# Performance work log

Hardware: AMD Instinct MI355X
Metric: run time of the kernel (lower is better)

## Reference

```python
import jax, jax.numpy as jnp
import numpy as np

_ALPHA_EPS = 1e-6


def _ema_weight_matrices(raw_alpha, T, dtype):
    """Return (K, T, T) row-normalized causal EMA weight matrices.

    W[k, t, s] = alpha_k^(t-s) / Z_t for s <= t, else 0, with Z_t the row sum.
    Computed in log space exactly like the torch reference.
    """
    alpha = jax.nn.sigmoid(raw_alpha).astype(dtype)
    alpha_safe = jnp.clip(alpha, _ALPHA_EPS, 1.0 - _ALPHA_EPS)  # (K,)
    idx = jnp.arange(T, dtype=dtype)
    diffs = idx[:, None] - idx[None, :]          # (T, T), t - s
    causal = diffs >= 0
    log_alpha = jnp.log(alpha_safe)              # (K,)
    log_W = log_alpha[:, None, None] * jnp.maximum(diffs, 0.0)  # (K, T, T)
    neg_inf = jnp.array(-jnp.inf, dtype=dtype)
    log_W = jnp.where(causal[None, :, :], log_W, neg_inf)
    log_Z = jax.nn.logsumexp(log_W, axis=2, keepdims=True)      # (K, T, 1)
    return jnp.exp(log_W - log_Z)                # (K, T, T)


def setup_inputs() -> dict:
    key = jax.random.key(0)
    k1, k2 = jax.random.split(key)
    B, T, d, K = 4, 4096, 512, 4
    h = jax.random.normal(k1, (B, T, d), dtype=jnp.float32)
    raw_alpha = jax.random.normal(k2, (K,), dtype=jnp.float32)
    return {"h": h, "raw_alpha": raw_alpha}


def reference(h, raw_alpha):
    """h: (B, T, d), raw_alpha: (K,) -> xis: (B, T, K, d)."""
    T = h.shape[1]
    W = _ema_weight_matrices(raw_alpha, T, h.dtype)   # (K, T, T)
    # per-channel causal weighted EMA: xi[b,t,k,:] = sum_s W[k,t,s] * h[b,s,:]
    return jnp.einsum('kts,bsd->btkd', W, h)
```

## Files before the change

### kernel.cpp

```cpp
#include <hip/hip_runtime.h>
#include <math.h>


namespace {

constexpr int T_LEN  = 4096;
constexpr int D_DIM  = 512;
constexpr int D4     = D_DIM / 4;
constexpr int K_CH   = 4;
constexpr int CHUNK  = 16;
constexpr int NCHUNK = T_LEN / CHUNK;
constexpr int GRP    = 16;
constexpr int NGRP   = NCHUNK / GRP;

typedef float floatx4 __attribute__((ext_vector_type(4)));

__device__ __forceinline__ float sigmoid_clip(float x) {
    float a = 1.0f / (1.0f + expf(-x));
    return fminf(fmaxf(a, 1e-6f), 1.0f - 1e-6f);
}

__device__ __forceinline__ void fma4(float4& d, float a, const float4& x) {
    d.x = fmaf(a, d.x, x.x);
    d.y = fmaf(a, d.y, x.y);
    d.z = fmaf(a, d.z, x.z);
    d.w = fmaf(a, d.w, x.w);
}

__device__ __forceinline__ void nt_store4(float4* p, const float4& v) {
    floatx4 nv;
    nv.x = v.x; nv.y = v.y; nv.z = v.z; nv.w = v.w;
    __builtin_nontemporal_store(nv, reinterpret_cast<floatx4*>(p));
}

__global__ void __launch_bounds__(128)
ema_chunk_sums(const float4* __restrict__ h4,
               const float*  __restrict__ raw_alpha,
               float4* __restrict__ lbuf) {
    const int c  = blockIdx.x % NCHUNK;
    const int b  = blockIdx.x / NCHUNK;
    const int d4 = threadIdx.x;

    float al[K_CH];
#pragma unroll
    for (int k = 0; k < K_CH; ++k) al[k] = sigmoid_clip(raw_alpha[k]);

    float4 acc[K_CH];
#pragma unroll
    for (int k = 0; k < K_CH; ++k) acc[k] = make_float4(0.f, 0.f, 0.f, 0.f);

    const float4* hp = h4 + ((size_t)b * T_LEN + (size_t)c * CHUNK) * D4 + d4;
#pragma unroll 4
    for (int j = 0; j < CHUNK; ++j) {
        const float4 hv = hp[(size_t)j * D4];
#pragma unroll
        for (int k = 0; k < K_CH; ++k) fma4(acc[k], al[k], hv);
    }
#pragma unroll
    for (int k = 0; k < K_CH; ++k)
        lbuf[(((size_t)b * NCHUNK + c) * K_CH + k) * D4 + d4] = acc[k];
}

__global__ void __launch_bounds__(128)
ema_group_sums(const float*  __restrict__ raw_alpha,
               const float4* __restrict__ lbuf,
               float4* __restrict__ gbuf) {
    const int g  = blockIdx.x % NGRP;
    const int b  = blockIdx.x / NGRP;
    const int d4 = threadIdx.x;

    float aC[K_CH];
#pragma unroll
    for (int k = 0; k < K_CH; ++k) {
        const float a = sigmoid_clip(raw_alpha[k]);
        aC[k] = exp2f((float)CHUNK * log2f(a));
    }

    float4 G[K_CH];
#pragma unroll
    for (int k = 0; k < K_CH; ++k) G[k] = make_float4(0.f, 0.f, 0.f, 0.f);

    const float4* lp = lbuf + (((size_t)b * NCHUNK + (size_t)g * GRP) * K_CH) * D4 + d4;
#pragma unroll 4
    for (int i = 0; i < GRP; ++i) {
#pragma unroll
        for (int k = 0; k < K_CH; ++k) {
            const float4 Lv = lp[((size_t)i * K_CH + k) * D4];
            fma4(G[k], aC[k], Lv);
        }
    }
#pragma unroll
    for (int k = 0; k < K_CH; ++k)
        gbuf[(((size_t)b * NGRP + g) * K_CH + k) * D4 + d4] = G[k];
}

__global__ void __launch_bounds__(128)
ema_apply(const float4* __restrict__ h4,
          const float*  __restrict__ raw_alpha,
          const float4* __restrict__ lbuf,
          const float4* __restrict__ gbuf,
          float4* __restrict__ out4) {
    const int c  = (NCHUNK - 1) - (blockIdx.x % NCHUNK);
    const int b  = blockIdx.x / NCHUNK;
    const int d4 = threadIdx.x;
    const int t0 = c * CHUNK;

    float al[K_CH], aC[K_CH], aG[K_CH];
#pragma unroll
    for (int k = 0; k < K_CH; ++k) {
        al[k] = sigmoid_clip(raw_alpha[k]);
        const float l2a = log2f(al[k]);
        aC[k] = exp2f((float)CHUNK * l2a);
        aG[k] = exp2f((float)(CHUNK * GRP) * l2a);
    }

    float4 S[K_CH];
#pragma unroll
    for (int k = 0; k < K_CH; ++k) S[k] = make_float4(0.f, 0.f, 0.f, 0.f);
    {
        const int g = c / GRP;
        const float4* gp = gbuf + ((size_t)b * NGRP * K_CH) * D4 + d4;
#pragma unroll 4
        for (int gq = 0; gq < g; ++gq) {
#pragma unroll
            for (int k = 0; k < K_CH; ++k) {
                const float4 Gv = gp[((size_t)gq * K_CH + k) * D4];
                fma4(S[k], aG[k], Gv);
            }
        }
        const float4* lp = lbuf + ((size_t)b * NCHUNK * K_CH) * D4 + d4;
#pragma unroll 4
        for (int cp = g * GRP; cp < c; ++cp) {
#pragma unroll
            for (int k = 0; k < K_CH; ++k) {
                const float4 Lv = lp[((size_t)cp * K_CH + k) * D4];
                fma4(S[k], aC[k], Lv);
            }
        }
    }

    float om[K_CH], pw[K_CH];
#pragma unroll
    for (int k = 0; k < K_CH; ++k) {
        om[k] = 1.0f - al[k];
        pw[k] = exp2f((float)(t0 + 1) * log2f(al[k]));
    }

    const float4* hp = h4 + ((size_t)b * T_LEN + t0) * D4 + d4;
    float4* op = out4 + (((size_t)b * T_LEN + t0) * (size_t)K_CH) * D4 + d4;

#pragma unroll 2
    for (int j = 0; j < CHUNK; ++j) {
        const float4 hv = hp[(size_t)j * D4];
#pragma unroll
        for (int k = 0; k < K_CH; ++k) {
            fma4(S[k], al[k], hv);
            const float invZ = om[k] / fmaxf(1.0f - pw[k], 1e-30f);
            float4 o;
            o.x = S[k].x * invZ;
            o.y = S[k].y * invZ;
            o.z = S[k].z * invZ;
            o.w = S[k].w * invZ;
            nt_store4(&op[((size_t)j * K_CH + k) * D4], o);
            pw[k] *= al[k];
        }
    }
}

}

extern "C" void kernel_launch(void* const* d_in, const int* in_sizes, int n_in,
                              void* d_out, int out_size, void* d_ws, size_t ws_size,
                              hipStream_t stream)
{
    const float4* h4        = (const float4*)d_in[0];
    const float*  raw_alpha = (const float*)d_in[1];
    float4* out4 = (float4*)d_out;

    const int B = in_sizes[0] / (T_LEN * D_DIM);

    float4* lbuf = (float4*)d_ws;
    float4* gbuf = lbuf + (size_t)B * NCHUNK * K_CH * D4;

    const dim3 blk(D4);

    hipLaunchKernelGGL(ema_chunk_sums, dim3(B * NCHUNK), blk, 0, stream,
                       h4, raw_alpha, lbuf);
    hipLaunchKernelGGL(ema_group_sums, dim3(B * NGRP), blk, 0, stream,
                       raw_alpha, lbuf, gbuf);
    hipLaunchKernelGGL(ema_apply, dim3(B * NCHUNK), blk, 0, stream,
                       h4, raw_alpha, lbuf, gbuf, out4);
}
```

Before: 53.74 us.

## Split chunk-prefix computation into separate kernel and retune chunk/group sizes

Moves the per-chunk carry-in prefix computation out of the output kernel into a new ema_chunk_prefix kernel that writes a prefix buffer, so the store-heavy apply kernel only loads one precomputed state per chunk. Chunk size doubles to 32 and group size halves to 8. Nontemporal stores are replaced by ordinary stores, and the apply grid is no longer reversed. This adds a fourth launch and extra workspace traffic in exchange for a lighter apply kernel.

```diff
diff --git a/kernel.cpp b/kernel.cpp
--- a/kernel.cpp
+++ b/kernel.cpp
@@ -8,12 +8,10 @@
 constexpr int D_DIM  = 512;
 constexpr int D4     = D_DIM / 4;
 constexpr int K_CH   = 4;
-constexpr int CHUNK  = 16;
+constexpr int CHUNK  = 32;
 constexpr int NCHUNK = T_LEN / CHUNK;
-constexpr int GRP    = 16;
+constexpr int GRP    = 8;
 constexpr int NGRP   = NCHUNK / GRP;
-
-typedef float floatx4 __attribute__((ext_vector_type(4)));
 
 __device__ __forceinline__ float sigmoid_clip(float x) {
     float a = 1.0f / (1.0f + expf(-x));
@@ -27,12 +25,6 @@
     d.w = fmaf(a, d.w, x.w);
 }
 
-__device__ __forceinline__ void nt_store4(float4* p, const float4& v) {
-    floatx4 nv;
-    nv.x = v.x; nv.y = v.y; nv.z = v.z; nv.w = v.w;
-    __builtin_nontemporal_store(nv, reinterpret_cast<floatx4*>(p));
-}
-
 __global__ void __launch_bounds__(128)
 ema_chunk_sums(const float4* __restrict__ h4,
                const float*  __restrict__ raw_alpha,
@@ -81,7 +73,7 @@
     for (int k = 0; k < K_CH; ++k) G[k] = make_float4(0.f, 0.f, 0.f, 0.f);
 
     const float4* lp = lbuf + (((size_t)b * NCHUNK + (size_t)g * GRP) * K_CH) * D4 + d4;
-#pragma unroll 4
+#pragma unroll
     for (int i = 0; i < GRP; ++i) {
 #pragma unroll
         for (int k = 0; k < K_CH; ++k) {
@@ -95,56 +87,72 @@
 }
 
 __global__ void __launch_bounds__(128)
+ema_chunk_prefix(const float*  __restrict__ raw_alpha,
+                 const float4* __restrict__ lbuf,
+                 const float4* __restrict__ gbuf,
+                 float4* __restrict__ pbuf) {
+    const int c  = blockIdx.x % NCHUNK;
+    const int b  = blockIdx.x / NCHUNK;
+    const int d4 = threadIdx.x;
+
+    float aC[K_CH], aG[K_CH];
+#pragma unroll
+    for (int k = 0; k < K_CH; ++k) {
+        const float a   = sigmoid_clip(raw_alpha[k]);
+        const float l2a = log2f(a);
+        aC[k] = exp2f((float)CHUNK * l2a);
+        aG[k] = exp2f((float)(CHUNK * GRP) * l2a);
+    }
+
+    float4 S[K_CH];
+#pragma unroll
+    for (int k = 0; k < K_CH; ++k) S[k] = make_float4(0.f, 0.f, 0.f, 0.f);
+
+    const int g = c / GRP;
+    const float4* gp = gbuf + ((size_t)b * NGRP * K_CH) * D4 + d4;
+    for (int gq = 0; gq < g; ++gq) {
+#pragma unroll
+        for (int k = 0; k < K_CH; ++k) {
+            const float4 Gv = gp[((size_t)gq * K_CH + k) * D4];
+            fma4(S[k], aG[k], Gv);
+        }
+    }
+    const float4* lp = lbuf + ((size_t)b * NCHUNK * K_CH) * D4 + d4;
+    for (int cp = g * GRP; cp < c; ++cp) {
+#pragma unroll
+        for (int k = 0; k < K_CH; ++k) {
+            const float4 Lv = lp[((size_t)cp * K_CH + k) * D4];
+            fma4(S[k], aC[k], Lv);
+        }
+    }
+#pragma unroll
+    for (int k = 0; k < K_CH; ++k)
+        pbuf[(((size_t)b * NCHUNK + c) * K_CH + k) * D4 + d4] = S[k];
+}
+
+__global__ void __launch_bounds__(128)
 ema_apply(const float4* __restrict__ h4,
           const float*  __restrict__ raw_alpha,
-          const float4* __restrict__ lbuf,
-          const float4* __restrict__ gbuf,
+          const float4* __restrict__ pbuf,
           float4* __restrict__ out4) {
-    const int c  = (NCHUNK - 1) - (blockIdx.x % NCHUNK);
+    const int c  = blockIdx.x % NCHUNK;
     const int b  = blockIdx.x / NCHUNK;
     const int d4 = threadIdx.x;
     const int t0 = c * CHUNK;
 
-    float al[K_CH], aC[K_CH], aG[K_CH];
+    float al[K_CH], om[K_CH], pw[K_CH];
 #pragma unroll
     for (int k = 0; k < K_CH; ++k) {
-        al[k] = sigmoid_clip(raw_alpha[k]);
-        const float l2a = log2f(al[k]);
-        aC[k] = exp2f((float)CHUNK * l2a);
-        aG[k] = exp2f((float)(CHUNK * GRP) * l2a);
+        const float a = sigmoid_clip(raw_alpha[k]);
+        al[k] = a;
+        om[k] = 1.0f - a;
+        pw[k] = exp2f((float)(t0 + 1) * log2f(a));
     }
 
     float4 S[K_CH];
 #pragma unroll
-    for (int k = 0; k < K_CH; ++k) S[k] = make_float4(0.f, 0.f, 0.f, 0.f);
-    {
-        const int g = c / GRP;
-        const float4* gp = gbuf + ((size_t)b * NGRP * K_CH) * D4 + d4;
-#pragma unroll 4
-        for (int gq = 0; gq < g; ++gq) {
-#pragma unroll
-            for (int k = 0; k < K_CH; ++k) {
-                const float4 Gv = gp[((size_t)gq * K_CH + k) * D4];
-                fma4(S[k], aG[k], Gv);
-            }
-        }
-        const float4* lp = lbuf + ((size_t)b * NCHUNK * K_CH) * D4 + d4;
-#pragma unroll 4
-        for (int cp = g * GRP; cp < c; ++cp) {
-#pragma unroll
-            for (int k = 0; k < K_CH; ++k) {
-                const float4 Lv = lp[((size_t)cp * K_CH + k) * D4];
-                fma4(S[k], aC[k], Lv);
-            }
-        }
-    }
-
-    float om[K_CH], pw[K_CH];
-#pragma unroll
-    for (int k = 0; k < K_CH; ++k) {
-        om[k] = 1.0f - al[k];
-        pw[k] = exp2f((float)(t0 + 1) * log2f(al[k]));
-    }
+    for (int k = 0; k < K_CH; ++k)
+        S[k] = pbuf[(((size_t)b * NCHUNK + c) * K_CH + k) * D4 + d4];
 
     const float4* hp = h4 + ((size_t)b * T_LEN + t0) * D4 + d4;
     float4* op = out4 + (((size_t)b * T_LEN + t0) * (size_t)K_CH) * D4 + d4;
@@ -161,7 +169,7 @@
             o.y = S[k].y * invZ;
             o.z = S[k].z * invZ;
             o.w = S[k].w * invZ;
-            nt_store4(&op[((size_t)j * K_CH + k) * D4], o);
+            op[((size_t)j * K_CH + k) * D4] = o;
             pw[k] *= al[k];
         }
     }
@@ -181,6 +189,7 @@
 
     float4* lbuf = (float4*)d_ws;
     float4* gbuf = lbuf + (size_t)B * NCHUNK * K_CH * D4;
+    float4* pbuf = gbuf + (size_t)B * NGRP   * K_CH * D4;
 
     const dim3 blk(D4);
 
@@ -188,6 +197,8 @@
                        h4, raw_alpha, lbuf);
     hipLaunchKernelGGL(ema_group_sums, dim3(B * NGRP), blk, 0, stream,
                        raw_alpha, lbuf, gbuf);
+    hipLaunchKernelGGL(ema_chunk_prefix, dim3(B * NCHUNK), blk, 0, stream,
+                       raw_alpha, lbuf, gbuf, pbuf);
     hipLaunchKernelGGL(ema_apply, dim3(B * NCHUNK), blk, 0, stream,
-                       h4, raw_alpha, lbuf, gbuf, out4);
-}
+                       h4, raw_alpha, pbuf, out4);
+}
```

New measurement: 51.74 us. 1.04x faster.
